# Performance work log

Measured on AMD Instinct MI355X. Metric: run time of the kernel, lower is better.

## Reference

```python
import jax, jax.numpy as jnp
import numpy as np

TOP_K = 512  # int(node_num * K) = int(2048 * 0.25)
NEG = -1.0e12
SLOPE = 0.01  # nn.LeakyReLU default negative_slope


def setup_inputs() -> dict:
    key = jax.random.key(0)
    k1, k2, k3, k4 = jax.random.split(key, 4)
    B, N, in_c, out_c, gs = 8, 2048, 128, 128, 128
    x = jax.random.normal(k1, (B, N, in_c), dtype=jnp.float32)
    W = jax.random.normal(k2, (in_c, out_c), dtype=jnp.float32) * (1.0 / np.sqrt(in_c))
    a = jax.random.normal(k3, (2 * out_c, 1), dtype=jnp.float32) * (1.0 / np.sqrt(2 * out_c))
    GL = jax.random.normal(k4, (N, gs), dtype=jnp.float32) * (1.0 / np.sqrt(gs))
    return {"x": x, "W": W, "a": a, "GL": GL}


def reference(x, W, a, GL):
    B, N, _ = x.shape
    out_c = W.shape[1]
    # learned adjacency: softmax(relu(GL GL^T)) + I  -> [N, N]
    adj = jax.nn.softmax(jax.nn.relu(GL @ GL.T), axis=-1) + jnp.eye(N, dtype=GL.dtype)
    h = x @ W  # [B, N, out_c]
    # e[b,i,j] = LeakyReLU( [h_i ; h_j] . a ) = LeakyReLU( h_i.a1 + h_j.a2 )
    # (avoids materializing the [B, N*N, 2*out_c] concat of the original)
    a1, a2 = a[:out_c, 0], a[out_c:, 0]
    e = jax.nn.leaky_relu((h @ a1)[:, :, None] + (h @ a2)[:, None, :], SLOPE)  # [B,N,N]
    att = jnp.where(adj[None] > 0, e, NEG)
    # top-k along dim=1 (rows, per column j): transpose so that axis is last
    att_t = jnp.swapaxes(att, 1, 2)  # [B, Nj, Ni]
    _, idx = jax.lax.top_k(att_t, TOP_K)  # idx: [B, Nj, TOP_K]
    b_ix = jnp.arange(B)[:, None, None]
    j_ix = jnp.arange(N)[None, :, None]
    mask_t = jnp.zeros_like(att_t).at[b_ix, j_ix, idx].set(1.0)
    mask = jnp.swapaxes(mask_t, 1, 2)  # [B, Ni, Nj]
    att = jax.nn.softmax(att * mask, axis=2)
    h_prime = jax.nn.relu(att @ h)  # [B, N, out_c]
    return jnp.swapaxes(h_prime, -2, -1)  # [B, out_c, N]
```

## Files before the change

kernel.cpp:

```cpp
#include <hip/hip_runtime.h>
#include <math.h>


#define B_ 8
#define N_ 2048
#define C_ 128
#define TOPK_ 512
#define NCH_ 32
#define CL_ 64
#define NP1_ 2052

#define P_OFF    ((size_t)0)
#define Q_OFF    (P_OFF + (size_t)B_*N_)
#define LOK_OFF  (Q_OFF + (size_t)B_*N_)
#define US_OFF   (LOK_OFF + (size_t)B_*N_)
#define VS_OFF   (US_OFF + (size_t)B_*N_)
#define SRT_OFF  (VS_OFF + (size_t)B_*N_)
#define SUS_OFF  (SRT_OFF + (size_t)B_*N_)
#define PVS_OFF  (SUS_OFF + (size_t)B_*NP1_)
#define SUX_OFF  (PVS_OFF + (size_t)B_*NP1_)
#define PVX_OFF  (SUX_OFF + (size_t)B_*N_*128)
#define TOTU_OFF (PVX_OFF + (size_t)B_*N_*128)
#define TOTV_OFF (TOTU_OFF + (size_t)B_*NCH_*128)
#define XPART_OFF (TOTV_OFF + (size_t)B_*NCH_*128)

__global__ __launch_bounds__(256) void k_pq(const float* __restrict__ x,
                                            const float* __restrict__ W,
                                            const float* __restrict__ a,
                                            float* __restrict__ p,
                                            float* __restrict__ q,
                                            float* __restrict__ xpart) {
  __shared__ float al[256];
  __shared__ float wa1[128], wa2[128];
  __shared__ float xps[2][128];
  const int t = threadIdx.x;
  const int r0 = blockIdx.x * 64;
  al[t] = a[t];
  __syncthreads();
  if (t < 128) {
    const float* Wr = W + (size_t)t * 128;
    float s1 = 0.f, s2 = 0.f;
#pragma unroll
    for (int j = 0; j < 128; j += 4) {
      float4 wv = *(const float4*)(Wr + j);
      s1 = fmaf(wv.x, al[j + 0], s1);
      s1 = fmaf(wv.y, al[j + 1], s1);
      s1 = fmaf(wv.z, al[j + 2], s1);
      s1 = fmaf(wv.w, al[j + 3], s1);
      s2 = fmaf(wv.x, al[128 + j + 0], s2);
      s2 = fmaf(wv.y, al[128 + j + 1], s2);
      s2 = fmaf(wv.z, al[128 + j + 2], s2);
      s2 = fmaf(wv.w, al[128 + j + 3], s2);
    }
    wa1[t] = s1; wa2[t] = s2;
  }
  __syncthreads();
  {
    const int row = t >> 2, part = t & 3;
    const float* xr = x + (size_t)(r0 + row) * 128 + part * 32;
    const float* w1 = wa1 + part * 32;
    const float* w2 = wa2 + part * 32;
    float sp = 0.f, sq = 0.f;
#pragma unroll
    for (int i = 0; i < 8; ++i) {
      float4 xv = *(const float4*)(xr + 4 * i);
      float4 w1v = *(const float4*)(w1 + 4 * i);
      float4 w2v = *(const float4*)(w2 + 4 * i);
      sp = fmaf(xv.x, w1v.x, sp); sp = fmaf(xv.y, w1v.y, sp);
      sp = fmaf(xv.z, w1v.z, sp); sp = fmaf(xv.w, w1v.w, sp);
      sq = fmaf(xv.x, w2v.x, sq); sq = fmaf(xv.y, w2v.y, sq);
      sq = fmaf(xv.z, w2v.z, sq); sq = fmaf(xv.w, w2v.w, sq);
    }
    sp += __shfl_xor(sp, 1, 64); sp += __shfl_xor(sp, 2, 64);
    sq += __shfl_xor(sq, 1, 64); sq += __shfl_xor(sq, 2, 64);
    if (part == 0) { p[r0 + row] = sp; q[r0 + row] = sq; }
  }
  {
    const int cc = t & 127, hh = t >> 7;
    float s = 0.f;
    for (int r2 = 32 * hh; r2 < 32 * hh + 32; ++r2)
      s += x[(size_t)(r0 + r2) * 128 + cc];
    xps[hh][cc] = s;
  }
  __syncthreads();
  if (t < 128)
    xpart[(size_t)blockIdx.x * 128 + t] = xps[0][t] + xps[1][t];
}

__global__ __launch_bounds__(256) void k_rank(const float* __restrict__ q,
                                              const float* __restrict__ p,
                                              float* __restrict__ u_s,
                                              float* __restrict__ v_s,
                                              int* __restrict__ srt,
                                              int* __restrict__ lok) {
  __shared__ float ql[N_], pl[N_];
  const int blk = blockIdx.x, t = threadIdx.x;
  const int b = blk >> 5, tile = blk & 31;
  const int i0 = tile * 64;
#pragma unroll
  for (int i = 0; i < 2; ++i) {
    ((float4*)ql)[t + 256 * i] = ((const float4*)(q + (size_t)b * N_))[t + 256 * i];
    ((float4*)pl)[t + 256 * i] = ((const float4*)(p + (size_t)b * N_))[t + 256 * i];
  }
  __syncthreads();
  const int row = t >> 2, s = t & 3;
  const int i = i0 + row;
  const float qi = ql[i], pi = pl[i];
  const float negpi = -pi;
  int qr = 0, lo = 0, pr = 0;
  for (int g = s; g < 512; g += 4) {
    float4 qj = ((const float4*)ql)[g];
    float4 pj = ((const float4*)pl)[g];
    const int j0 = 4 * g;
    qr += (qj.x < qi || (qj.x == qi && (j0 + 0) < i)) ? 1 : 0;
    qr += (qj.y < qi || (qj.y == qi && (j0 + 1) < i)) ? 1 : 0;
    qr += (qj.z < qi || (qj.z == qi && (j0 + 2) < i)) ? 1 : 0;
    qr += (qj.w < qi || (qj.w == qi && (j0 + 3) < i)) ? 1 : 0;
    lo += (qj.x < negpi) ? 1 : 0;
    lo += (qj.y < negpi) ? 1 : 0;
    lo += (qj.z < negpi) ? 1 : 0;
    lo += (qj.w < negpi) ? 1 : 0;
    pr += (pj.x > pi || (pj.x == pi && (j0 + 0) < i)) ? 1 : 0;
    pr += (pj.y > pi || (pj.y == pi && (j0 + 1) < i)) ? 1 : 0;
    pr += (pj.z > pi || (pj.z == pi && (j0 + 2) < i)) ? 1 : 0;
    pr += (pj.w > pi || (pj.w == pi && (j0 + 3) < i)) ? 1 : 0;
  }
  qr += __shfl_xor(qr, 1, 64); qr += __shfl_xor(qr, 2, 64);
  lo += __shfl_xor(lo, 1, 64); lo += __shfl_xor(lo, 2, 64);
  pr += __shfl_xor(pr, 1, 64); pr += __shfl_xor(pr, 2, 64);
  if (s == 0) {
    u_s[(size_t)b * N_ + qr] = __expf(qi);
    v_s[(size_t)b * N_ + qr] = __expf(0.01f * qi);
    srt[(size_t)b * N_ + qr] = i;
    lok[(size_t)b * N_ + i] = lo | ((pr < TOPK_) ? 0x10000 : 0);
  }
}

__global__ __launch_bounds__(256) void k_scan(const float* __restrict__ x,
                                              const float* __restrict__ u_s,
                                              const float* __restrict__ v_s,
                                              const int* __restrict__ srt,
                                              float* __restrict__ SUX,
                                              float* __restrict__ PVX,
                                              float* __restrict__ totU,
                                              float* __restrict__ totV,
                                              float* __restrict__ SUS,
                                              float* __restrict__ PVS) {
  __shared__ float hl[CL_][128];
  __shared__ float ul[CL_], vl[CL_];
  __shared__ int sl[CL_];
  __shared__ float2 sa[256], sb[256];
  const int t = threadIdx.x;
  if (blockIdx.x >= 256) {
    const int b = blockIdx.x - 256;
    float4 ua = ((const float4*)(u_s + (size_t)b * N_))[2 * t];
    float4 ub = ((const float4*)(u_s + (size_t)b * N_))[2 * t + 1];
    float4 wa = ((const float4*)(v_s + (size_t)b * N_))[2 * t];
    float4 wb = ((const float4*)(v_s + (size_t)b * N_))[2 * t + 1];
    float su = ua.x + ua.y + ua.z + ua.w + ub.x + ub.y + ub.z + ub.w;
    float sw = wa.x + wa.y + wa.z + wa.w + wb.x + wb.y + wb.z + wb.w;
    sa[t] = make_float2(su, sw);
    __syncthreads();
    float2* cur = sa; float2* nxt = sb;
    for (int off = 1; off < 256; off <<= 1) {
      float2 vv = cur[t];
      if (t >= off) { float2 o = cur[t - off]; vv.x += o.x; vv.y += o.y; }
      nxt[t] = vv;
      __syncthreads();
      float2* tmp = cur; cur = nxt; nxt = tmp;
    }
    float2 incl = cur[t];
    float2 tot = cur[255];
    float exclU = incl.x - su, exclW = incl.y - sw;
    float s0 = tot.x - exclU;
    float s1 = s0 - ua.x, s2 = s1 - ua.y, s3 = s2 - ua.z;
    float s4 = s3 - ua.w, s5 = s4 - ub.x, s6 = s5 - ub.y, s7 = s6 - ub.z;
    float p0 = exclW;
    float p1 = p0 + wa.x, p2 = p1 + wa.y, p3 = p2 + wa.z;
    float p4 = p3 + wa.w, p5 = p4 + wb.x, p6 = p5 + wb.y, p7 = p6 + wb.z;
    float* Sb = SUS + (size_t)b * NP1_ + 8 * t;
    float* Pb = PVS + (size_t)b * NP1_ + 8 * t;
    *(float4*)(Sb) = make_float4(s0, s1, s2, s3);
    *(float4*)(Sb + 4) = make_float4(s4, s5, s6, s7);
    *(float4*)(Pb) = make_float4(p0, p1, p2, p3);
    *(float4*)(Pb + 4) = make_float4(p4, p5, p6, p7);
    if (t == 255) {
      SUS[(size_t)b * NP1_ + N_] = 0.f;
      PVS[(size_t)b * NP1_ + N_] = tot.y;
    }
    return;
  }
  const int b = blockIdx.x >> 5, ch = blockIdx.x & 31;
  const int base = b * N_ + ch * CL_;
  if (t < CL_) { ul[t] = u_s[base + t]; vl[t] = v_s[base + t]; sl[t] = srt[base + t]; }
  __syncthreads();
  {
    const int c4 = t & 31, rr = t >> 5;
#pragma unroll
    for (int i = 0; i < 8; ++i) {
      int tt = rr + 8 * i;
      float4 v = *(const float4*)(x + ((size_t)b * N_ + sl[tt]) * 128 + 4 * c4);
      *(float4*)(&hl[tt][4 * c4]) = v;
    }
  }
  __syncthreads();
  if (t < 128) {
    const int c = t;
    float run = 0.f;
    for (int tt = CL_ - 1; tt >= 0; --tt) {
      run = fmaf(ul[tt], hl[tt][c], run);
      SUX[((size_t)(base + tt)) * 128 + c] = run;
    }
    totU[(size_t)(b * NCH_ + ch) * 128 + c] = run;
  } else {
    const int c = t - 128;
    float run2 = 0.f;
    for (int tt = 0; tt < CL_; ++tt) {
      PVX[((size_t)(base + tt)) * 128 + c] = run2;
      run2 = fmaf(vl[tt], hl[tt][c], run2);
    }
    totV[(size_t)(b * NCH_ + ch) * 128 + c] = run2;
  }
}

__global__ __launch_bounds__(256) void k_out(const float* __restrict__ p,
                                             const int* __restrict__ lok,
                                             const float* __restrict__ SUS,
                                             const float* __restrict__ PVS,
                                             const float* __restrict__ SUX,
                                             const float* __restrict__ PVX,
                                             const float* __restrict__ totU,
                                             const float* __restrict__ totV,
                                             const float* __restrict__ xpart,
                                             const float* __restrict__ W,
                                             float* __restrict__ out) {
  __shared__ float Wl[128 * 128];
  __shared__ float zl[64 * 132];
  __shared__ union {
    struct { float CSU[(NCH_ + 1) * 128]; float CPV[(NCH_ + 1) * 128]; float xm[128]; } tb;
    float res[64 * 129];
  } u_;
  __shared__ float A_s[64], B_s[64], invD[64];
  __shared__ int lo_s[64], keep_s[64];
  const int b = blockIdx.x >> 5, tile = blockIdx.x & 31;
  const int t = threadIdx.x;
  const int i0 = tile * 64;
  {
    const float4* W4 = (const float4*)W;
    float4* Wl4 = (float4*)Wl;
#pragma unroll
    for (int i = 0; i < 16; ++i) Wl4[t + 256 * i] = W4[t + 256 * i];
  }
  if (t < 128) {
    float ms = 0.f;
#pragma unroll
    for (int j = 0; j < 32; ++j) ms += xpart[(size_t)(b * 32 + j) * 128 + t];
    u_.tb.xm[t] = ms * (1.0f / (float)N_);
    float s = 0.f;
    u_.tb.CSU[NCH_ * 128 + t] = 0.f;
    for (int cc = NCH_ - 1; cc >= 0; --cc) {
      s += totU[(size_t)(b * NCH_ + cc) * 128 + t];
      u_.tb.CSU[cc * 128 + t] = s;
    }
  } else {
    const int c2 = t - 128;
    float s2 = 0.f;
    for (int cc = 0; cc < NCH_; ++cc) {
      u_.tb.CPV[cc * 128 + c2] = s2;
      s2 += totV[(size_t)(b * NCH_ + cc) * 128 + c2];
    }
    u_.tb.CPV[NCH_ * 128 + c2] = s2;
  }
  __syncthreads();
  if (t < 64) {
    float pv = p[b * N_ + i0 + t];
    int lk = lok[(size_t)b * N_ + i0 + t];
    keep_s[t] = (lk >> 16) & 1;
    int lo = lk & 0xFFFF;
    lo_s[t] = lo;
    float A = __expf(pv), Bv = __expf(0.01f * pv);
    A_s[t] = A; B_s[t] = Bv;
    float sus = SUS[(size_t)b * NP1_ + lo];
    float pvs = PVS[(size_t)b * NP1_ + lo];
    invD[t] = 1.0f / fmaf(A, sus, Bv * pvs);
  }
  __syncthreads();
  {
    const int half = t >> 7, c = t & 127;
#pragma unroll 4
    for (int ii2 = 0; ii2 < 64; ii2 += 2) {
      int ii = ii2 + half;
      float zv;
      if (keep_s[ii]) {
        int lo = lo_s[ii];
        float A = A_s[ii], Bv = B_s[ii];
        float suc, pvc;
        if (lo < N_) {
          int chn = lo >> 6;
          size_t ro = ((size_t)(b * N_ + lo)) * 128;
          suc = SUX[ro + c] + u_.tb.CSU[(chn + 1) * 128 + c];
          pvc = PVX[ro + c] + u_.tb.CPV[chn * 128 + c];
        } else {
          suc = 0.f;
          pvc = u_.tb.CPV[NCH_ * 128 + c];
        }
        zv = fmaf(A, suc, Bv * pvc) * invD[ii];
      } else {
        zv = u_.tb.xm[c];
      }
      zl[ii * 132 + c] = zv;
    }
  }
  __syncthreads();
  const int cg = t & 15, rp = t >> 4;
  float acc[4][8];
#pragma unroll
  for (int r = 0; r < 4; ++r)
#pragma unroll
    for (int j = 0; j < 8; ++j) acc[r][j] = 0.f;
  for (int k = 0; k < 128; ++k) {
    const float4* Wr = (const float4*)(Wl + k * 128);
    float4 w0 = Wr[cg];
    float4 w1 = Wr[cg + 16];
#pragma unroll
    for (int r = 0; r < 4; ++r) {
      float zv = zl[(4 * rp + r) * 132 + k];
      acc[r][0] = fmaf(zv, w0.x, acc[r][0]);
      acc[r][1] = fmaf(zv, w0.y, acc[r][1]);
      acc[r][2] = fmaf(zv, w0.z, acc[r][2]);
      acc[r][3] = fmaf(zv, w0.w, acc[r][3]);
      acc[r][4] = fmaf(zv, w1.x, acc[r][4]);
      acc[r][5] = fmaf(zv, w1.y, acc[r][5]);
      acc[r][6] = fmaf(zv, w1.z, acc[r][6]);
      acc[r][7] = fmaf(zv, w1.w, acc[r][7]);
    }
  }
  __syncthreads();
  {
    const int c0 = 4 * cg, c1 = 4 * cg + 64;
#pragma unroll
    for (int r = 0; r < 4; ++r) {
      int row = 4 * rp + r;
#pragma unroll
      for (int j = 0; j < 4; ++j) {
        u_.res[row * 129 + c0 + j] = fmaxf(acc[r][j], 0.f);
        u_.res[row * 129 + c1 + j] = fmaxf(acc[r][4 + j], 0.f);
      }
    }
  }
  __syncthreads();
#pragma unroll
  for (int pass = 0; pass < 8; ++pass) {
    int cc = (t >> 4) + pass * 16;
    int ii4 = (t & 15) * 4;
    float4 v;
    v.x = u_.res[(ii4 + 0) * 129 + cc];
    v.y = u_.res[(ii4 + 1) * 129 + cc];
    v.z = u_.res[(ii4 + 2) * 129 + cc];
    v.w = u_.res[(ii4 + 3) * 129 + cc];
    *(float4*)(out + ((size_t)(b * C_ + cc)) * N_ + i0 + ii4) = v;
  }
}

extern "C" void kernel_launch(void* const* d_in, const int* in_sizes, int n_in,
                              void* d_out, int out_size, void* d_ws, size_t ws_size,
                              hipStream_t stream) {
  (void)in_sizes; (void)n_in; (void)out_size; (void)ws_size;
  const float* x = (const float*)d_in[0];
  const float* W = (const float*)d_in[1];
  const float* a = (const float*)d_in[2];
  float* out = (float*)d_out;
  float* ws = (float*)d_ws;

  float* p    = ws + P_OFF;
  float* q    = ws + Q_OFF;
  int*   lok  = (int*)(ws + LOK_OFF);
  float* u_s  = ws + US_OFF;
  float* v_s  = ws + VS_OFF;
  int*   srt  = (int*)(ws + SRT_OFF);
  float* SUS  = ws + SUS_OFF;
  float* PVS  = ws + PVS_OFF;
  float* SUX  = ws + SUX_OFF;
  float* PVX  = ws + PVX_OFF;
  float* totU = ws + TOTU_OFF;
  float* totV = ws + TOTV_OFF;
  float* xpart = ws + XPART_OFF;

  k_pq<<<dim3((B_ * N_) / 64), dim3(256), 0, stream>>>(x, W, a, p, q, xpart);
  k_rank<<<dim3(B_ * 32), dim3(256), 0, stream>>>(q, p, u_s, v_s, srt, lok);
  k_scan<<<dim3(256 + B_), dim3(256), 0, stream>>>(x, u_s, v_s, srt, SUX, PVX, totU, totV, SUS, PVS);
  k_out<<<dim3(B_ * 32), dim3(256), 0, stream>>>(p, lok, SUS, PVS, SUX, PVX, totU, totV, xpart, W, out);
}
```

Baseline: 118.5 us.

## Split k_out into 16-row tiles and read W from global memory

The output kernel now handles 16 rows per block instead of 64, so it launches four times as many blocks (1024 versus 256) to fill more compute units. The 64KB shared-memory copy of W is removed and W is read straight from global memory or cache inside the GEMM loop, which cuts shared-memory use and raises occupancy. The cost is that every block rebuilds the per-batch CSU/CPV prefix tables and the xm mean, four times as many blocks in total. Each thread now computes one row times 8 columns, so there is less register reuse of W.

```diff
diff --git a/kernel.cpp b/kernel.cpp
--- a/kernel.cpp
+++ b/kernel.cpp
@@ -234,23 +234,16 @@
                                              const float* __restrict__ xpart,
                                              const float* __restrict__ W,
                                              float* __restrict__ out) {
-  __shared__ float Wl[128 * 128];
-  __shared__ float zl[64 * 132];
+  __shared__ float zl[16 * 132];
   __shared__ union {
     struct { float CSU[(NCH_ + 1) * 128]; float CPV[(NCH_ + 1) * 128]; float xm[128]; } tb;
-    float res[64 * 129];
+    float res[16 * 129];
   } u_;
-  __shared__ float A_s[64], B_s[64], invD[64];
-  __shared__ int lo_s[64], keep_s[64];
-  const int b = blockIdx.x >> 5, tile = blockIdx.x & 31;
+  __shared__ float A_s[16], B_s[16], invD[16];
+  __shared__ int lo_s[16], keep_s[16];
+  const int b = blockIdx.x >> 7, tile = blockIdx.x & 127;
   const int t = threadIdx.x;
-  const int i0 = tile * 64;
-  {
-    const float4* W4 = (const float4*)W;
-    float4* Wl4 = (float4*)Wl;
-#pragma unroll
-    for (int i = 0; i < 16; ++i) Wl4[t + 256 * i] = W4[t + 256 * i];
-  }
+  const int i0 = tile * 16;
   if (t < 128) {
     float ms = 0.f;
 #pragma unroll
@@ -272,7 +265,7 @@
     u_.tb.CPV[NCH_ * 128 + c2] = s2;
   }
   __syncthreads();
-  if (t < 64) {
+  if (t < 16) {
     float pv = p[b * N_ + i0 + t];
     int lk = lok[(size_t)b * N_ + i0 + t];
     keep_s[t] = (lk >> 16) & 1;
@@ -287,9 +280,9 @@
   __syncthreads();
   {
     const int half = t >> 7, c = t & 127;
-#pragma unroll 4
-    for (int ii2 = 0; ii2 < 64; ii2 += 2) {
-      int ii = ii2 + half;
+#pragma unroll
+    for (int m = 0; m < 8; ++m) {
+      int ii = 2 * m + half;
       float zv;
       if (keep_s[ii]) {
         int lo = lo_s[ii];
@@ -312,47 +305,40 @@
     }
   }
   __syncthreads();
-  const int cg = t & 15, rp = t >> 4;
-  float acc[4][8];
-#pragma unroll
-  for (int r = 0; r < 4; ++r)
-#pragma unroll
-    for (int j = 0; j < 8; ++j) acc[r][j] = 0.f;
-  for (int k = 0; k < 128; ++k) {
-    const float4* Wr = (const float4*)(Wl + k * 128);
-    float4 w0 = Wr[cg];
-    float4 w1 = Wr[cg + 16];
-#pragma unroll
-    for (int r = 0; r < 4; ++r) {
-      float zv = zl[(4 * rp + r) * 132 + k];
-      acc[r][0] = fmaf(zv, w0.x, acc[r][0]);
-      acc[r][1] = fmaf(zv, w0.y, acc[r][1]);
-      acc[r][2] = fmaf(zv, w0.z, acc[r][2]);
-      acc[r][3] = fmaf(zv, w0.w, acc[r][3]);
-      acc[r][4] = fmaf(zv, w1.x, acc[r][4]);
-      acc[r][5] = fmaf(zv, w1.y, acc[r][5]);
-      acc[r][6] = fmaf(zv, w1.z, acc[r][6]);
-      acc[r][7] = fmaf(zv, w1.w, acc[r][7]);
-    }
-  }
-  __syncthreads();
-  {
-    const int c0 = 4 * cg, c1 = 4 * cg + 64;
-#pragma unroll
-    for (int r = 0; r < 4; ++r) {
-      int row = 4 * rp + r;
-#pragma unroll
-      for (int j = 0; j < 4; ++j) {
-        u_.res[row * 129 + c0 + j] = fmaxf(acc[r][j], 0.f);
-        u_.res[row * 129 + c1 + j] = fmaxf(acc[r][4 + j], 0.f);
-      }
-    }
-  }
-  __syncthreads();
-#pragma unroll
-  for (int pass = 0; pass < 8; ++pass) {
-    int cc = (t >> 4) + pass * 16;
-    int ii4 = (t & 15) * 4;
+  const int cg = t & 15, row = t >> 4;
+  const int c0 = 4 * cg, c1 = 4 * cg + 64;
+  float acc[8];
+#pragma unroll
+  for (int j = 0; j < 8; ++j) acc[j] = 0.f;
+  {
+    const float4* W4 = (const float4*)W;
+#pragma unroll 4
+    for (int k = 0; k < 128; ++k) {
+      float4 w0 = W4[k * 32 + cg];
+      float4 w1 = W4[k * 32 + cg + 16];
+      float zv = zl[row * 132 + k];
+      acc[0] = fmaf(zv, w0.x, acc[0]);
+      acc[1] = fmaf(zv, w0.y, acc[1]);
+      acc[2] = fmaf(zv, w0.z, acc[2]);
+      acc[3] = fmaf(zv, w0.w, acc[3]);
+      acc[4] = fmaf(zv, w1.x, acc[4]);
+      acc[5] = fmaf(zv, w1.y, acc[5]);
+      acc[6] = fmaf(zv, w1.z, acc[6]);
+      acc[7] = fmaf(zv, w1.w, acc[7]);
+    }
+  }
+  __syncthreads();
+#pragma unroll
+  for (int j = 0; j < 4; ++j) {
+    u_.res[row * 129 + c0 + j] = fmaxf(acc[j], 0.f);
+    u_.res[row * 129 + c1 + j] = fmaxf(acc[4 + j], 0.f);
+  }
+  __syncthreads();
+#pragma unroll
+  for (int pass = 0; pass < 2; ++pass) {
+    int idx = pass * 256 + t;
+    int cc = idx >> 2;
+    int ii4 = (idx & 3) * 4;
     float4 v;
     v.x = u_.res[(ii4 + 0) * 129 + cc];
     v.y = u_.res[(ii4 + 1) * 129 + cc];
@@ -389,5 +375,5 @@
   k_pq<<<dim3((B_ * N_) / 64), dim3(256), 0, stream>>>(x, W, a, p, q, xpart);
   k_rank<<<dim3(B_ * 32), dim3(256), 0, stream>>>(q, p, u_s, v_s, srt, lok);
   k_scan<<<dim3(256 + B_), dim3(256), 0, stream>>>(x, u_s, v_s, srt, SUX, PVX, totU, totV, SUS, PVS);
-  k_out<<<dim3(B_ * 32), dim3(256), 0, stream>>>(p, lok, SUS, PVS, SUX, PVX, totU, totV, xpart, W, out);
-}
+  k_out<<<dim3(B_ * 128), dim3(256), 0, stream>>>(p, lok, SUS, PVS, SUX, PVX, totU, totV, xpart, W, out);
+}
```

Result: slower. 140.4 us (+18.4%).
